# Kernel tuning notes

Hardware: AMD Instinct MI355X
Metric: run time of the kernel (lower is better)

## Reference

```python
import jax, jax.numpy as jnp
import numpy as np

D = 1024      # dim_input
H = 16        # n_heads
DH = 64       # dim_inner
S = 1024      # current_seq
M = 1024      # pre_seq (memory)
B = 2         # batch
SCALE = 1.0 / np.sqrt(DH)


def _rel_shift(x):
    # x: [S, J, B, H]; Transformer-XL relative shift
    s, j = x.shape[0], x.shape[1]
    zero = jnp.zeros((s, 1) + x.shape[2:], x.dtype)
    x = jnp.concatenate([zero, x], axis=1)            # [S, J+1, B, H]
    x = x.reshape((j + 1, s) + x.shape[2:])[1:]        # [J, S, B, H]
    return x.reshape((s, j) + x.shape[2:])             # [S, J, B, H]


def setup_inputs() -> dict:
    key = jax.random.key(0)
    ks = jax.random.split(key, 9)
    std = 1.0 / np.sqrt(D)
    return {
        "multi_head_input": jax.random.normal(ks[0], (S, B, D), jnp.float32),
        "position_emb": jax.random.normal(ks[1], (S + M, D), jnp.float32),
        "memory": jax.random.normal(ks[2], (M, B, D), jnp.float32),
        "u": jax.random.normal(ks[3], (H, DH), jnp.float32) * 0.02,
        "v": jax.random.normal(ks[4], (H, DH), jnp.float32) * 0.02,
        "W_kv": jax.random.normal(ks[5], (D, 2 * H * DH), jnp.float32) * std,
        "W_q": jax.random.normal(ks[6], (D, H * DH), jnp.float32) * std,
        "W_pos": jax.random.normal(ks[7], (D, H * DH), jnp.float32) * std,
        "W_out": jax.random.normal(ks[8], (H * DH, D), jnp.float32) * std,
    }


def reference(multi_head_input, position_emb, memory, u, v, W_kv, W_q, W_pos, W_out):
    s = multi_head_input.shape[0]
    m = memory.shape[0]
    b = multi_head_input.shape[1]
    x_mem = jnp.concatenate([memory, multi_head_input], axis=0)   # [M+S, B, D]
    kv = x_mem @ W_kv                                              # [M+S, B, 2*H*DH]
    k, val = jnp.split(kv, 2, axis=-1)
    k = k.reshape(m + s, b, H, DH)
    val = val.reshape(m + s, b, H, DH)
    q = (multi_head_input @ W_q).reshape(s, b, H, DH)              # [S, B, H, DH]

    # content term: (q + u) . k
    content = jnp.einsum('ibhd,jbhd->ijbh', q + u, k)              # [S, M+S, B, H]
    # position term: (q + v) . r, then rel_shift
    r = (position_emb @ W_pos).reshape(m + s, H, DH)               # [M+S, H, DH]
    pos = jnp.einsum('ibhd,jhd->ijbh', q + v, r)                   # [S, M+S, B, H]
    pos = _rel_shift(pos)

    attn = jax.nn.softmax((content + pos) * SCALE, axis=1)         # [S, M+S, B, H]
    out = jnp.einsum('ijbh,jbhd->ibhd', attn, val).reshape(s, b, H * DH)
    return out @ W_out                                             # [S, B, D]
```

## Files before the change

### kernel.cpp

```cpp
#include <hip/hip_runtime.h>
#include <hip/hip_bf16.h>
#include <hip/hip_fp16.h>
#include <math.h>

#define D    1024
#define H    16
#define DH   64
#define S    1024
#define M    1024
#define B    2
#define J    2048
#define SCALE 0.125f

typedef __attribute__((ext_vector_type(8))) short        bf16x8;
typedef __attribute__((ext_vector_type(4))) short        s16x4;
typedef __attribute__((ext_vector_type(8))) _Float16     h16x8;
typedef __attribute__((ext_vector_type(4))) _Float16     h16x4;
typedef __attribute__((ext_vector_type(8))) unsigned short us8;
typedef __attribute__((ext_vector_type(4))) float        f32x4;

__device__ __forceinline__ short f2bs(float f) {
    __hip_bfloat16 t = __float2bfloat16(f);
    short r; __builtin_memcpy(&r, &t, 2); return r;
}
__device__ __forceinline__ unsigned short f2bf_fast(float f) {
    unsigned int u; __builtin_memcpy(&u, &f, 4);
    return (unsigned short)((u + 0x8000u) >> 16);
}

__device__ __forceinline__ void g2l16(const short* g, short* l) {
    __builtin_amdgcn_global_load_lds(
        (const __attribute__((address_space(1))) unsigned int*)g,
        (__attribute__((address_space(3))) unsigned int*)l, 16, 0, 0);
}

__global__ __launch_bounds__(256)
void prep(const float* __restrict__ mem, const float* __restrict__ x,
          const float* __restrict__ pemb,
          const float* __restrict__ Wkv, const float* __restrict__ Wq,
          const float* __restrict__ Wpos, const float* __restrict__ Wout,
          short* __restrict__ a_bf, short* __restrict__ p_bf,
          short* __restrict__ wkvt, short* __restrict__ wqt,
          short* __restrict__ wpt,  short* __restrict__ wot)
{
    __shared__ float t[64][65];
    int blk = blockIdx.x;
    const int tid = threadIdx.x;
    if (blk < 6144) {
        const int idx = (blk * 256 + tid) * 4;
        const int TWO_M = 2 * 1024 * 1024;
        float4 v; short* dst;
        if (idx < TWO_M)          { v = *(const float4*)(mem  + idx);           dst = a_bf + idx; }
        else if (idx < 2 * TWO_M) { v = *(const float4*)(x    + idx - TWO_M);   dst = a_bf + idx; }
        else                      { v = *(const float4*)(pemb + idx - 2*TWO_M); dst = p_bf + idx - 2*TWO_M; }
        s16x4 o = { f2bs(v.x), f2bs(v.y), f2bs(v.z), f2bs(v.w) };
        *(s16x4*)dst = o;
        return;
    }
    blk -= 6144;
    const float* src; short* dst; int N, t0;
    if (blk < 512)       { src = Wkv;  dst = wkvt; N = 2048; t0 = blk; }
    else if (blk < 768)  { src = Wq;   dst = wqt;  N = 1024; t0 = blk - 512; }
    else if (blk < 1024) { src = Wpos; dst = wpt;  N = 1024; t0 = blk - 768; }
    else                 { src = Wout; dst = wot;  N = 1024; t0 = blk - 1024; }
    const int ntn = N >> 6;
    const int k0 = (t0 / ntn) * 64, n0 = (t0 % ntn) * 64;
    #pragma unroll
    for (int e = tid; e < 4096; e += 256) {
        int r = e >> 6, c = e & 63;
        t[r][c] = src[(size_t)(k0 + r) * N + n0 + c];
    }
    __syncthreads();
    #pragma unroll
    for (int e = tid; e < 4096; e += 256) {
        int nr = e >> 6, kc = e & 63;
        dst[(size_t)(n0 + nr) * 1024 + k0 + kc] = f2bs(t[kc][nr]);
    }
}

__device__ __forceinline__ void gemm_core(const short* __restrict__ A,
                                          const short* __restrict__ Bt,
                                          short* As, short* Bs,
                                          int bm0, int bn0, int tid,
                                          f32x4 acc[4][4])
{
    const int w    = tid >> 6;
    const int wy   = w >> 1, wx = w & 1;
    const int lane = tid & 63;
    const int lm   = lane & 15;
    const int lq   = lane >> 4;

    for (int k0 = 0; k0 < 1024; k0 += 64) {
        const short* Ab = A  + (size_t)bm0 * 1024 + k0;
        const short* Bb = Bt + (size_t)bn0 * 1024 + k0;
        #pragma unroll
        for (int t = 0; t < 4; ++t) {
            int s = t * 256 + tid;
            int r = s >> 3, c = s & 7;
            int cg = c ^ (r & 7);
            g2l16(Ab + r * 1024 + cg * 8, As + s * 8);
            g2l16(Bb + r * 1024 + cg * 8, Bs + s * 8);
        }
        __syncthreads();
        #pragma unroll
        for (int kk = 0; kk < 2; ++kk) {
            bf16x8 af[4], bg[4];
            #pragma unroll
            for (int r4 = 0; r4 < 4; ++r4) {
                int ar = wy * 64 + r4 * 16 + lm;
                int kc = kk * 4 + lq;
                af[r4] = *(const bf16x8*)(As + ((ar << 3) + (kc ^ (ar & 7))) * 8);
            }
            #pragma unroll
            for (int c4 = 0; c4 < 4; ++c4) {
                int br = wx * 64 + c4 * 16 + lm;
                int kc = kk * 4 + lq;
                bg[c4] = *(const bf16x8*)(Bs + ((br << 3) + (kc ^ (br & 7))) * 8);
            }
            #pragma unroll
            for (int r4 = 0; r4 < 4; ++r4)
                #pragma unroll
                for (int c4 = 0; c4 < 4; ++c4)
                    acc[r4][c4] = __builtin_amdgcn_mfma_f32_16x16x32_bf16(
                        af[r4], bg[c4], acc[r4][c4], 0, 0, 0);
        }
        __syncthreads();
    }
}

__global__ __launch_bounds__(256)
void proj_fused(const short* __restrict__ a_bf, const short* __restrict__ p_bf,
                const short* __restrict__ wkvt, const short* __restrict__ wqt,
                const short* __restrict__ wpt,
                short* __restrict__ k_bf, short* __restrict__ vt_bf,
                short* __restrict__ qu_bf, short* __restrict__ qv_bf,
                short* __restrict__ r_bf,
                const float* __restrict__ uvec, const float* __restrict__ vvec)
{
    __shared__ __align__(16) short As[128 * 64];
    __shared__ __align__(16) short Bs[128 * 64];

    int blk = blockIdx.x;
    int mode, bx, by;
    const short *A, *Bt;
    if (blk < 512)      { bx = blk & 15; by = blk >> 4;
                          if (bx >= 8) { mode = 4; A = wkvt; Bt = a_bf; }
                          else         { mode = 0; A = a_bf; Bt = wkvt; } }
    else if (blk < 640) { int b2 = blk - 512; mode = 1; bx = b2 & 7; by = b2 >> 3;
                          A = a_bf + (size_t)2048 * 1024; Bt = wqt; }
    else                { int b3 = blk - 640; mode = 2; bx = b3 & 7; by = b3 >> 3;
                          A = p_bf; Bt = wpt; }
    const int bn0 = (mode == 4) ? by * 128 : bx * 128;
    const int bm0 = (mode == 4) ? bx * 128 : by * 128;
    const int tid = threadIdx.x;
    const int w = tid >> 6, wy = w >> 1, wx = w & 1;
    const int lane = tid & 63, lm = lane & 15, lq = lane >> 4;

    f32x4 acc[4][4];
    #pragma unroll
    for (int r = 0; r < 4; ++r)
        #pragma unroll
        for (int c = 0; c < 4; ++c) acc[r][c] = (f32x4){0.f, 0.f, 0.f, 0.f};

    gemm_core(A, Bt, As, Bs, bm0, bn0, tid, acc);

    #pragma unroll
    for (int r4 = 0; r4 < 4; ++r4) {
        #pragma unroll
        for (int c4 = 0; c4 < 4; ++c4) {
            const int n = bn0 + wx * 64 + c4 * 16 + lm;
            float ubias = 0.f, vbias = 0.f;
            if (mode == 1) { ubias = uvec[n]; vbias = vvec[n]; }
            #pragma unroll
            for (int reg = 0; reg < 4; ++reg) {
                const int m = bm0 + wy * 64 + r4 * 16 + lq * 4 + reg;
                const float val = acc[r4][c4][reg];
                if (mode == 0) {
                    int j = m >> 1, b = m & 1;
                    int h = n >> 6, d = n & 63;
                    k_bf[(((size_t)b * H + h) * J + j) * DH + d] = f2bs(val);
                } else if (mode == 4) {
                    int n2 = m - 1024, h = n2 >> 6, d = n2 & 63;
                    int j = n >> 1, b = n & 1;
                    vt_bf[(((size_t)b * H + h) * DH + d) * J + j] = f2bs(val);
                } else if (mode == 1) {
                    int i = m >> 1, b = m & 1;
                    int h = n >> 6, d = n & 63;
                    size_t o = (((size_t)b * H + h) * S + i) * DH + d;
                    qu_bf[o] = f2bs((val + ubias) * SCALE);
                    qv_bf[o] = f2bs((val + vbias) * SCALE);
                } else {
                    int h = n >> 6, d = n & 63;
                    r_bf[((size_t)h * J + m) * DH + d] = f2bs(val);
                }
            }
        }
    }
}

__global__ __launch_bounds__(256)
void gemm_out(const short* __restrict__ A, const short* __restrict__ Bt,
              float* __restrict__ out)
{
    __shared__ __align__(16) short As[128 * 64];
    __shared__ __align__(16) short Bs[128 * 64];
    const int bn0 = blockIdx.x * 128, bm0 = blockIdx.y * 128;
    const int tid = threadIdx.x;
    const int w = tid >> 6, wy = w >> 1, wx = w & 1;
    const int lane = tid & 63, lm = lane & 15, lq = lane >> 4;

    f32x4 acc[4][4];
    #pragma unroll
    for (int r = 0; r < 4; ++r)
        #pragma unroll
        for (int c = 0; c < 4; ++c) acc[r][c] = (f32x4){0.f, 0.f, 0.f, 0.f};

    gemm_core(A, Bt, As, Bs, bm0, bn0, tid, acc);

    #pragma unroll
    for (int r4 = 0; r4 < 4; ++r4)
        #pragma unroll
        for (int c4 = 0; c4 < 4; ++c4) {
            const int n = bn0 + wx * 64 + c4 * 16 + lm;
            #pragma unroll
            for (int reg = 0; reg < 4; ++reg) {
                const int m = bm0 + wy * 64 + r4 * 16 + lq * 4 + reg;
                out[(size_t)m * 1024 + n] = acc[r4][c4][reg];
            }
        }
}

__device__ __forceinline__ int sidx(int m, int c) {
    return (m << 10) + (c ^ (m << 3));
}

__global__ __launch_bounds__(512)
void attn_mfma(const short* __restrict__ qu_bf, const short* __restrict__ qv_bf,
               const short* __restrict__ k_bf,  const short* __restrict__ vt_bf,
               const short* __restrict__ r_bf,
               float* __restrict__ opart, float* __restrict__ ml)
{
    __shared__ unsigned short sc[32 * 1024];
    __half* sch = (__half*)sc;
    float*  scF = (float*)sc;

    const int bh  = blockIdx.x;
    const int it  = blockIdx.y;
    const int jh  = blockIdx.z;
    const int i0  = it * 32;
    const int cbeg = jh << 10, cend = cbeg + 1024;
    const int h   = bh & (H - 1);
    const int tid = threadIdx.x;
    const int w    = tid >> 6;
    const int lane = tid & 63;
    const int lm   = lane & 15;
    const int lq   = lane >> 4;
    const int slot = (it * 32 + bh) * 2 + jh;

    const short* qup0 = qu_bf + ((size_t)(bh * S + i0 + lm)) * DH + lq * 8;
    const short* qup1 = qup0 + 16 * DH;
    bf16x8 au00 = *(const bf16x8*)qup0,        au01 = *(const bf16x8*)(qup0 + 32);
    bf16x8 au10 = *(const bf16x8*)qup1,        au11 = *(const bf16x8*)(qup1 + 32);
    const short* qvp0 = qv_bf + ((size_t)(bh * S + i0 + lm)) * DH + lq * 8;
    const short* qvp1 = qvp0 + 16 * DH;
    bf16x8 av00 = *(const bf16x8*)qvp0,        av01 = *(const bf16x8*)(qvp0 + 32);
    bf16x8 av10 = *(const bf16x8*)qvp1,        av11 = *(const bf16x8*)(qvp1 + 32);
    int r1a = i0 + 1 + lm;  if (r1a > S - 1) r1a = S - 1;
    int r1b = i0 + 17 + lm; if (r1b > S - 1) r1b = S - 1;
    const short* qwp0 = qv_bf + ((size_t)(bh * S + r1a)) * DH + lq * 8;
    const short* qwp1 = qv_bf + ((size_t)(bh * S + r1b)) * DH + lq * 8;
    bf16x8 aw00 = *(const bf16x8*)qwp0,        aw01 = *(const bf16x8*)(qwp0 + 32);
    bf16x8 aw10 = *(const bf16x8*)qwp1,        aw11 = *(const bf16x8*)(qwp1 + 32);

    if (tid < 32) {
        int hole = i0 + tid + 1025;
        if (hole >= cbeg && hole < cend) sc[sidx(tid, hole - cbeg)] = 0;
    }

    const short* rbase = r_bf + (size_t)h * J * DH;

    {
        int tmp = cbeg + 977 - i0;
        int tlo = tmp > 0 ? ((tmp + 15) >> 4) : 0;
        int thi = (cend + 1022 - i0) >> 4; if (thi > 127) thi = 127;
        int t = tlo + w;
        if (t <= thi) {
            const short* rp = rbase + (size_t)(t * 16 + lm) * DH + lq * 8;
            bf16x8 b0 = *(const bf16x8*)rp, b1 = *(const bf16x8*)(rp + 32);
            for (; t <= thi; t += 8) {
                bf16x8 n0, n1;
                if (t + 8 <= thi) {
                    const short* rpn = rbase + (size_t)((t + 8) * 16 + lm) * DH + lq * 8;
                    n0 = *(const bf16x8*)rpn; n1 = *(const bf16x8*)(rpn + 32);
                }
                f32x4 c0 = {0.f,0.f,0.f,0.f}, c1 = {0.f,0.f,0.f,0.f};
                c0 = __builtin_amdgcn_mfma_f32_16x16x32_bf16(av00, b0, c0, 0, 0, 0);
                c1 = __builtin_amdgcn_mfma_f32_16x16x32_bf16(av10, b0, c1, 0, 0, 0);
                c0 = __builtin_amdgcn_mfma_f32_16x16x32_bf16(av01, b1, c0, 0, 0, 0);
                c1 = __builtin_amdgcn_mfma_f32_16x16x32_bf16(av11, b1, c1, 0, 0, 0);
                int cb = i0 + t * 16 + lm - 1023 - cbeg;
                int base = i0 + 16 * t - 1023;
                if (base >= cbeg && base + 46 < cend) {
                    #pragma unroll
                    for (int r = 0; r < 4; ++r) {
                        int m0 = lq * 4 + r, m1 = m0 + 16;
                        sch[sidx(m0, cb + m0)] = __float2half(c0[r]);
                        sch[sidx(m1, cb + m1)] = __float2half(c1[r]);
                    }
                } else {
                    #pragma unroll
                    for (int r = 0; r < 4; ++r) {
                        int m0 = lq * 4 + r, m1 = m0 + 16;
                        int cA = cb + m0, cB = cb + m1;
                        if (cA >= 0 && cA < 1024) sch[sidx(m0, cA)] = __float2half(c0[r]);
                        if (cB >= 0 && cB < 1024) sch[sidx(m1, cB)] = __float2half(c1[r]);
                    }
                }
                b0 = n0; b1 = n1;
            }
        }
    }

    {
        int tmpw = cbeg - 1072 - i0;
        int tlw = tmpw > 0 ? ((tmpw + 15) >> 4) : 0;
        int thw = (cend - 1027 - i0) >> 4; if (thw > 127) thw = 127;
        int t = tlw + w;
        if (t <= thw) {
            const short* rp = rbase + (size_t)(t * 16 + lm) * DH + lq * 8;
            bf16x8 b0 = *(const bf16x8*)rp, b1 = *(const bf16x8*)(rp + 32);
            for (; t <= thw; t += 8) {
                bf16x8 n0, n1;
                if (t + 8 <= thw) {
                    const short* rpn = rbase + (size_t)((t + 8) * 16 + lm) * DH + lq * 8;
                    n0 = *(const bf16x8*)rpn; n1 = *(const bf16x8*)(rpn + 32);
                }
                f32x4 c0 = {0.f,0.f,0.f,0.f}, c1 = {0.f,0.f,0.f,0.f};
                c0 = __builtin_amdgcn_mfma_f32_16x16x32_bf16(aw00, b0, c0, 0, 0, 0);
                c1 = __builtin_amdgcn_mfma_f32_16x16x32_bf16(aw10, b0, c1, 0, 0, 0);
                c0 = __builtin_amdgcn_mfma_f32_16x16x32_bf16(aw01, b1, c0, 0, 0, 0);
                c1 = __builtin_amdgcn_mfma_f32_16x16x32_bf16(aw11, b1, c1, 0, 0, 0);
                int cb = i0 + t * 16 + lm + 1026 - cbeg;
                int base = i0 + 16 * t + 1026;
                if (base >= cbeg && base + 46 < cend) {
                    #pragma unroll
                    for (int r = 0; r < 4; ++r) {
                        int m0 = lq * 4 + r, m1 = m0 + 16;
                        sch[sidx(m0, cb + m0)] = __float2half(c0[r]);
                        sch[sidx(m1, cb + m1)] = __float2half(c1[r]);
                    }
                } else {
                    #pragma unroll
                    for (int r = 0; r < 4; ++r) {
                        int m0 = lq * 4 + r, m1 = m0 + 16;
                        int cA = cb + m0, cB = cb + m1;
                        if (cA >= 0 && cA < 1024) sch[sidx(m0, cA)] = __float2half(c0[r]);
                        if (cB >= 0 && cB < 1024) sch[sidx(m1, cB)] = __float2half(c1[r]);
                    }
                }
                b0 = n0; b1 = n1;
            }
        }
    }

    const short* kbase = k_bf + (size_t)bh * J * DH;
    int tc0 = jh * 64 + w + 8 * (it & 7);
    const short* kp0 = kbase + (size_t)(tc0 * 16 + lm) * DH + lq * 8;
    bf16x8 kb0 = *(const bf16x8*)kp0, kb1 = *(const bf16x8*)(kp0 + 32);
    __syncthreads();

    #pragma unroll 1
    for (int g = 0; g < 8; ++g) {
        bf16x8 nb0, nb1;
        if (g + 1 < 8) {
            int u = jh * 64 + w + 8 * ((g + 1 + it) & 7);
            const short* np = kbase + (size_t)(u * 16 + lm) * DH + lq * 8;
            nb0 = *(const bf16x8*)np; nb1 = *(const bf16x8*)(np + 32);
        }
        int t = jh * 64 + w + 8 * ((g + it) & 7);
        int lc = t * 16 - cbeg;
        int aA = sidx(lm,      lc + lq * 4);
        int aB = sidx(lm + 16, lc + lq * 4);
        h16x4 hA = *(const h16x4*)(sc + aA);
        h16x4 hB = *(const h16x4*)(sc + aB);
        f32x4 c0, c1;
        #pragma unroll
        for (int r = 0; r < 4; ++r) { c0[r] = (float)hA[r]; c1[r] = (float)hB[r]; }
        c0 = __builtin_amdgcn_mfma_f32_16x16x32_bf16(kb0, au00, c0, 0, 0, 0);
        c1 = __builtin_amdgcn_mfma_f32_16x16x32_bf16(kb0, au10, c1, 0, 0, 0);
        c0 = __builtin_amdgcn_mfma_f32_16x16x32_bf16(kb1, au01, c0, 0, 0, 0);
        c1 = __builtin_amdgcn_mfma_f32_16x16x32_bf16(kb1, au11, c1, 0, 0, 0);
        h16x4 oA, oB;
        #pragma unroll
        for (int r = 0; r < 4; ++r) { oA[r] = (_Float16)c0[r]; oB[r] = (_Float16)c1[r]; }
        *(h16x4*)(sc + aA) = oA;
        *(h16x4*)(sc + aB) = oB;
        kb0 = nb0; kb1 = nb1;
    }

    const int dslice = w & 3, jq = w >> 2;
    const short* vtb = vt_bf + ((size_t)bh * DH + dslice * 16 + lm) * J + cbeg + jq * 512;
    bf16x8 cv0, cv1, cv2, cv3;
    {
        int j0 = (it & 3) * 128;
        cv0 = *(const bf16x8*)(vtb + j0 +  0 + lq * 8);
        cv1 = *(const bf16x8*)(vtb + j0 + 32 + lq * 8);
        cv2 = *(const bf16x8*)(vtb + j0 + 64 + lq * 8);
        cv3 = *(const bf16x8*)(vtb + j0 + 96 + lq * 8);
    }
    __syncthreads();

    {
        const int row = tid >> 4;
        const int cw  = (tid & 15) * 8;
        float ssum = 0.f;
        #pragma unroll
        for (int c = cw; c < 1024; c += 128) {
            int idx = sidx(row, c);
            h16x8 v = *(const h16x8*)(sc + idx);
            us8 e;
            #pragma unroll
            for (int k = 0; k < 8; ++k) {
                float ex = __builtin_amdgcn_exp2f((float)v[k] * 1.44269504f);
                ssum += ex;
                e[k] = f2bf_fast(ex);
            }
            *(us8*)(sc + idx) = e;
        }
        #pragma unroll
        for (int off = 1; off < 16; off <<= 1) ssum += __shfl_xor(ssum, off);
        if ((tid & 15) == 0) {
            ml[(size_t)slot * 64 + row * 2]     = 0.f;
            ml[(size_t)slot * 64 + row * 2 + 1] = ssum;
        }
    }
    __syncthreads();

    f32x4 pa0 = {0.f,0.f,0.f,0.f}, pa1 = {0.f,0.f,0.f,0.f};
    f32x4 pa2 = {0.f,0.f,0.f,0.f}, pa3 = {0.f,0.f,0.f,0.f};
    f32x4 pb0 = {0.f,0.f,0.f,0.f}, pb1 = {0.f,0.f,0.f,0.f};
    f32x4 pb2 = {0.f,0.f,0.f,0.f}, pb3 = {0.f,0.f,0.f,0.f};
    #pragma unroll 1
    for (int jo0 = 0; jo0 < 4; ++jo0) {
        bf16x8 nv0, nv1, nv2, nv3;
        if (jo0 < 3) {
            int jn = ((jo0 + 1 + it) & 3) * 128;
            nv0 = *(const bf16x8*)(vtb + jn +  0 + lq * 8);
            nv1 = *(const bf16x8*)(vtb + jn + 32 + lq * 8);
            nv2 = *(const bf16x8*)(vtb + jn + 64 + lq * 8);
            nv3 = *(const bf16x8*)(vtb + jn + 96 + lq * 8);
        }
        int j0 = ((jo0 + it) & 3) * 128;
        int lb = jq * 512 + j0;
        bf16x8 a0 = *(const bf16x8*)(sc + sidx(lm, lb +  0 + lq * 8));
        bf16x8 a1 = *(const bf16x8*)(sc + sidx(lm, lb + 32 + lq * 8));
        bf16x8 a2 = *(const bf16x8*)(sc + sidx(lm, lb + 64 + lq * 8));
        bf16x8 a3 = *(const bf16x8*)(sc + sidx(lm, lb + 96 + lq * 8));
        bf16x8 c0 = *(const bf16x8*)(sc + sidx(16 + lm, lb +  0 + lq * 8));
        bf16x8 c1 = *(const bf16x8*)(sc + sidx(16 + lm, lb + 32 + lq * 8));
        bf16x8 c2 = *(const bf16x8*)(sc + sidx(16 + lm, lb + 64 + lq * 8));
        bf16x8 c3 = *(const bf16x8*)(sc + sidx(16 + lm, lb + 96 + lq * 8));
        pa0 = __builtin_amdgcn_mfma_f32_16x16x32_bf16(a0, cv0, pa0, 0, 0, 0);
        pb0 = __builtin_amdgcn_mfma_f32_16x16x32_bf16(c0, cv0, pb0, 0, 0, 0);
        pa1 = __builtin_amdgcn_mfma_f32_16x16x32_bf16(a1, cv1, pa1, 0, 0, 0);
        pb1 = __builtin_amdgcn_mfma_f32_16x16x32_bf16(c1, cv1, pb1, 0, 0, 0);
        pa2 = __builtin_amdgcn_mfma_f32_16x16x32_bf16(a2, cv2, pa2, 0, 0, 0);
        pb2 = __builtin_amdgcn_mfma_f32_16x16x32_bf16(c2, cv2, pb2, 0, 0, 0);
        pa3 = __builtin_amdgcn_mfma_f32_16x16x32_bf16(a3, cv3, pa3, 0, 0, 0);
        pb3 = __builtin_amdgcn_mfma_f32_16x16x32_bf16(c3, cv3, pb3, 0, 0, 0);
        if (jo0 < 3) { cv0 = nv0; cv1 = nv1; cv2 = nv2; cv3 = nv3; }
    }
    __syncthreads();

    #pragma unroll
    for (int r = 0; r < 4; ++r) {
        int m0 = lq * 4 + r, m1 = m0 + 16;
        scF[jq * 2048 + m0 * 64 + dslice * 16 + lm] = pa0[r] + pa1[r] + pa2[r] + pa3[r];
        scF[jq * 2048 + m1 * 64 + dslice * 16 + lm] = pb0[r] + pb1[r] + pb2[r] + pb3[r];
    }
    __syncthreads();

    float* op = opart + (size_t)slot * 2048;
    #pragma unroll
    for (int e = tid; e < 2048; e += 512)
        op[e] = scF[e] + scF[2048 + e];
}

__global__ __launch_bounds__(256)
void attn_combine(const float* __restrict__ opart, const float* __restrict__ ml,
                  short* __restrict__ o_bf)
{
    const int blk = blockIdx.x;
    const int it = blk >> 5, bh = blk & 31;
    const int h = bh & 15, b = bh >> 4;
    __shared__ float wgt[32][2];
    const int tid = threadIdx.x;
    if (tid < 32) {
        float m0 = ml[(size_t)(blk * 2 + 0) * 64 + tid * 2];
        float l0 = ml[(size_t)(blk * 2 + 0) * 64 + tid * 2 + 1];
        float m1 = ml[(size_t)(blk * 2 + 1) * 64 + tid * 2];
        float l1 = ml[(size_t)(blk * 2 + 1) * 64 + tid * 2 + 1];
        float mx = fmaxf(m0, m1);
        float e0 = __expf(m0 - mx), e1 = __expf(m1 - mx);
        float inv = 1.0f / (e0 * l0 + e1 * l1);
        wgt[tid][0] = e0 * inv;
        wgt[tid][1] = e1 * inv;
    }
    __syncthreads();
    const float* p0 = opart + (size_t)(blk * 2 + 0) * 2048;
    const float* p1 = opart + (size_t)(blk * 2 + 1) * 2048;
    #pragma unroll
    for (int e = tid; e < 2048; e += 256) {
        int m = e >> 6, d = e & 63;
        float val = p0[e] * wgt[m][0] + p1[e] * wgt[m][1];
        o_bf[((size_t)(it * 32 + m) * B + b) * (H * DH) + h * DH + d] = f2bs(val);
    }
}

extern "C" void kernel_launch(void* const* d_in, const int* in_sizes, int n_in,
                              void* d_out, int out_size, void* d_ws, size_t ws_size,
                              hipStream_t stream)
{
    const float* x    = (const float*)d_in[0];
    const float* pemb = (const float*)d_in[1];
    const float* mem  = (const float*)d_in[2];
    const float* u    = (const float*)d_in[3];
    const float* v    = (const float*)d_in[4];
    const float* Wkv  = (const float*)d_in[5];
    const float* Wq   = (const float*)d_in[6];
    const float* Wpos = (const float*)d_in[7];
    const float* Wout = (const float*)d_in[8];
    float* out = (float*)d_out;

    char* p = (char*)d_ws;
    short* a_bf  = (short*)p; p += (size_t)4096 * 1024 * 2;
    short* p_bf  = (short*)p; p += (size_t)2048 * 1024 * 2;
    short* wkvt  = (short*)p; p += (size_t)2048 * 1024 * 2;
    short* wqt   = (short*)p; p += (size_t)1024 * 1024 * 2;
    short* wpt   = (short*)p; p += (size_t)1024 * 1024 * 2;
    short* wot   = (short*)p; p += (size_t)1024 * 1024 * 2;
    short* k_bf  = (short*)p; p += (size_t)B * H * J * DH * 2;
    short* vt_bf = (short*)p; p += (size_t)B * H * J * DH * 2;
    short* qu_bf = (short*)p; p += (size_t)B * H * S * DH * 2;
    short* qv_bf = (short*)p; p += (size_t)B * H * S * DH * 2;
    short* r_bf  = (short*)p; p += (size_t)H * J * DH * 2;
    short* o_bf  = (short*)p;

    float* opart = (float*)d_ws;
    float* ml    = (float*)((char*)d_ws + (size_t)16 * 1024 * 1024);

    prep<<<7424, 256, 0, stream>>>(mem, x, pemb, Wkv, Wq, Wpos, Wout,
                                   a_bf, p_bf, wkvt, wqt, wpt, wot);
    proj_fused<<<768, 256, 0, stream>>>(a_bf, p_bf, wkvt, wqt, wpt,
                                        k_bf, vt_bf, qu_bf, qv_bf, r_bf, u, v);
    attn_mfma<<<dim3(B * H, S / 32, 2), 512, 0, stream>>>(
        qu_bf, qv_bf, k_bf, vt_bf, r_bf, opart, ml);
    attn_combine<<<(S / 32) * B * H, 256, 0, stream>>>(opart, ml, o_bf);
    gemm_out<<<dim3(8, 16), 256, 0, stream>>>(o_bf, wot, out);
}
```

Measured before the change: 296.4 us.

## Process attention key range in two 512-column chunks to halve score LDS

New measurement: 320.6 us. 1.08x slower.

```diff
diff --git a/kernel.cpp b/kernel.cpp
--- a/kernel.cpp
+++ b/kernel.cpp
@@ -231,7 +231,7 @@
 }
 
 __device__ __forceinline__ int sidx(int m, int c) {
-    return (m << 10) + (c ^ (m << 3));
+    return (m << 9) + (c ^ (m << 3));
 }
 
 __global__ __launch_bounds__(512)
@@ -240,15 +240,14 @@
                const short* __restrict__ r_bf,
                float* __restrict__ opart, float* __restrict__ ml)
 {
-    __shared__ unsigned short sc[32 * 1024];
+    __shared__ __align__(16) unsigned short sc[32 * 512];
+    __shared__ __align__(16) float oacc[4096];
     __half* sch = (__half*)sc;
-    float*  scF = (float*)sc;
 
     const int bh  = blockIdx.x;
     const int it  = blockIdx.y;
     const int jh  = blockIdx.z;
     const int i0  = it * 32;
-    const int cbeg = jh << 10, cend = cbeg + 1024;
     const int h   = bh & (H - 1);
     const int tid = threadIdx.x;
     const int w    = tid >> 6;
@@ -256,234 +255,259 @@
     const int lm   = lane & 15;
     const int lq   = lane >> 4;
     const int slot = (it * 32 + bh) * 2 + jh;
-
-    const short* qup0 = qu_bf + ((size_t)(bh * S + i0 + lm)) * DH + lq * 8;
-    const short* qup1 = qup0 + 16 * DH;
-    bf16x8 au00 = *(const bf16x8*)qup0,        au01 = *(const bf16x8*)(qup0 + 32);
-    bf16x8 au10 = *(const bf16x8*)qup1,        au11 = *(const bf16x8*)(qup1 + 32);
-    const short* qvp0 = qv_bf + ((size_t)(bh * S + i0 + lm)) * DH + lq * 8;
-    const short* qvp1 = qvp0 + 16 * DH;
-    bf16x8 av00 = *(const bf16x8*)qvp0,        av01 = *(const bf16x8*)(qvp0 + 32);
-    bf16x8 av10 = *(const bf16x8*)qvp1,        av11 = *(const bf16x8*)(qvp1 + 32);
-    int r1a = i0 + 1 + lm;  if (r1a > S - 1) r1a = S - 1;
-    int r1b = i0 + 17 + lm; if (r1b > S - 1) r1b = S - 1;
-    const short* qwp0 = qv_bf + ((size_t)(bh * S + r1a)) * DH + lq * 8;
-    const short* qwp1 = qv_bf + ((size_t)(bh * S + r1b)) * DH + lq * 8;
-    bf16x8 aw00 = *(const bf16x8*)qwp0,        aw01 = *(const bf16x8*)(qwp0 + 32);
-    bf16x8 aw10 = *(const bf16x8*)qwp1,        aw11 = *(const bf16x8*)(qwp1 + 32);
-
-    if (tid < 32) {
-        int hole = i0 + tid + 1025;
-        if (hole >= cbeg && hole < cend) sc[sidx(tid, hole - cbeg)] = 0;
-    }
+    const int dslice = w & 3, jq = w >> 2;
 
     const short* rbase = r_bf + (size_t)h * J * DH;
+    const short* kbase = k_bf + (size_t)bh * J * DH;
+
+    float ssum = 0.f;
+
+    #pragma unroll 1
+    for (int ch = 0; ch < 2; ++ch) {
+        const int cbeg = (jh << 10) + (ch << 9);
+        const int cend = cbeg + 512;
+
+        const short* qvp0 = qv_bf + ((size_t)(bh * S + i0 + lm)) * DH + lq * 8;
+        const short* qvp1 = qvp0 + 16 * DH;
+        bf16x8 av00 = *(const bf16x8*)qvp0, av01 = *(const bf16x8*)(qvp0 + 32);
+        bf16x8 av10 = *(const bf16x8*)qvp1, av11 = *(const bf16x8*)(qvp1 + 32);
+        int r1a = i0 + 1 + lm;  if (r1a > S - 1) r1a = S - 1;
+        int r1b = i0 + 17 + lm; if (r1b > S - 1) r1b = S - 1;
+        const short* qwp0 = qv_bf + ((size_t)(bh * S + r1a)) * DH + lq * 8;
+        const short* qwp1 = qv_bf + ((size_t)(bh * S + r1b)) * DH + lq * 8;
+        bf16x8 aw00 = *(const bf16x8*)qwp0, aw01 = *(const bf16x8*)(qwp0 + 32);
+        bf16x8 aw10 = *(const bf16x8*)qwp1, aw11 = *(const bf16x8*)(qwp1 + 32);
+
+        if (tid < 32) {
+            int hole = i0 + tid + 1025;
+            if (hole >= cbeg && hole < cend) sc[sidx(tid, hole - cbeg)] = 0;
+        }
+
+        {
+            int tmp = cbeg + 977 - i0;
+            int tlo = tmp > 0 ? ((tmp + 15) >> 4) : 0;
+            int thi = (cend + 1022 - i0) >> 4; if (thi > 127) thi = 127;
+            int t = tlo + w;
+            if (t <= thi) {
+                const short* rp = rbase + (size_t)(t * 16 + lm) * DH + lq * 8;
+                bf16x8 b0 = *(const bf16x8*)rp, b1 = *(const bf16x8*)(rp + 32);
+                for (; t <= thi; t += 8) {
+                    bf16x8 n0, n1;
+                    if (t + 8 <= thi) {
+                        const short* rpn = rbase + (size_t)((t + 8) * 16 + lm) * DH + lq * 8;
+                        n0 = *(const bf16x8*)rpn; n1 = *(const bf16x8*)(rpn + 32);
+                    }
+                    f32x4 c0 = {0.f,0.f,0.f,0.f}, c1 = {0.f,0.f,0.f,0.f};
+                    c0 = __builtin_amdgcn_mfma_f32_16x16x32_bf16(av00, b0, c0, 0, 0, 0);
+                    c1 = __builtin_amdgcn_mfma_f32_16x16x32_bf16(av10, b0, c1, 0, 0, 0);
+                    c0 = __builtin_amdgcn_mfma_f32_16x16x32_bf16(av01, b1, c0, 0, 0, 0);
+                    c1 = __builtin_amdgcn_mfma_f32_16x16x32_bf16(av11, b1, c1, 0, 0, 0);
+                    int cb = i0 + t * 16 + lm - 1023 - cbeg;
+                    int base = i0 + 16 * t - 1023;
+                    if (base >= cbeg && base + 46 < cend) {
+                        #pragma unroll
+                        for (int r = 0; r < 4; ++r) {
+                            int m0 = lq * 4 + r, m1 = m0 + 16;
+                            sch[sidx(m0, cb + m0)] = __float2half(c0[r]);
+                            sch[sidx(m1, cb + m1)] = __float2half(c1[r]);
+                        }
+                    } else {
+                        #pragma unroll
+                        for (int r = 0; r < 4; ++r) {
+                            int m0 = lq * 4 + r, m1 = m0 + 16;
+                            int cA = cb + m0, cB = cb + m1;
+                            if (cA >= 0 && cA < 512) sch[sidx(m0, cA)] = __float2half(c0[r]);
+                            if (cB >= 0 && cB < 512) sch[sidx(m1, cB)] = __float2half(c1[r]);
+                        }
+                    }
+                    b0 = n0; b1 = n1;
+                }
+            }
+        }
+
+        {
+            int tmpw = cbeg - 1072 - i0;
+            int tlw = tmpw > 0 ? ((tmpw + 15) >> 4) : 0;
+            int thw = (cend - 1027 - i0) >> 4; if (thw > 127) thw = 127;
+            int t = tlw + w;
+            if (t <= thw) {
+                const short* rp = rbase + (size_t)(t * 16 + lm) * DH + lq * 8;
+                bf16x8 b0 = *(const bf16x8*)rp, b1 = *(const bf16x8*)(rp + 32);
+                for (; t <= thw; t += 8) {
+                    bf16x8 n0, n1;
+                    if (t + 8 <= thw) {
+                        const short* rpn = rbase + (size_t)((t + 8) * 16 + lm) * DH + lq * 8;
+                        n0 = *(const bf16x8*)rpn; n1 = *(const bf16x8*)(rpn + 32);
+                    }
+                    f32x4 c0 = {0.f,0.f,0.f,0.f}, c1 = {0.f,0.f,0.f,0.f};
+                    c0 = __builtin_amdgcn_mfma_f32_16x16x32_bf16(aw00, b0, c0, 0, 0, 0);
+                    c1 = __builtin_amdgcn_mfma_f32_16x16x32_bf16(aw10, b0, c1, 0, 0, 0);
+                    c0 = __builtin_amdgcn_mfma_f32_16x16x32_bf16(aw01, b1, c0, 0, 0, 0);
+                    c1 = __builtin_amdgcn_mfma_f32_16x16x32_bf16(aw11, b1, c1, 0, 0, 0);
+                    int cb = i0 + t * 16 + lm + 1026 - cbeg;
+                    int base = i0 + 16 * t + 1026;
+                    if (base >= cbeg && base + 46 < cend) {
+                        #pragma unroll
+                        for (int r = 0; r < 4; ++r) {
+                            int m0 = lq * 4 + r, m1 = m0 + 16;
+                            sch[sidx(m0, cb + m0)] = __float2half(c0[r]);
+                            sch[sidx(m1, cb + m1)] = __float2half(c1[r]);
+                        }
+                    } else {
+                        #pragma unroll
+                        for (int r = 0; r < 4; ++r) {
+                            int m0 = lq * 4 + r, m1 = m0 + 16;
+                            int cA = cb + m0, cB = cb + m1;
+                            if (cA >= 0 && cA < 512) sch[sidx(m0, cA)] = __float2half(c0[r]);
+                            if (cB >= 0 && cB < 512) sch[sidx(m1, cB)] = __float2half(c1[r]);
+                        }
+                    }
+                    b0 = n0; b1 = n1;
+                }
+            }
+        }
+
+        const int tb = cbeg >> 4;
+        bf16x8 kb0, kb1;
+        {
+            int t0 = tb + w + 8 * (it & 3);
+            const short* kp0 = kbase + (size_t)(t0 * 16 + lm) * DH + lq * 8;
+            kb0 = *(const bf16x8*)kp0; kb1 = *(const bf16x8*)(kp0 + 32);
+        }
+        __syncthreads();
+
+        const short* qup0 = qu_bf + ((size_t)(bh * S + i0 + lm)) * DH + lq * 8;
+        const short* qup1 = qup0 + 16 * DH;
+        bf16x8 au00 = *(const bf16x8*)qup0, au01 = *(const bf16x8*)(qup0 + 32);
+        bf16x8 au10 = *(const bf16x8*)qup1, au11 = *(const bf16x8*)(qup1 + 32);
+
+        #pragma unroll 1
+        for (int g = 0; g < 4; ++g) {
+            bf16x8 nb0, nb1;
+            if (g + 1 < 4) {
+                int u = tb + w + 8 * ((g + 1 + it) & 3);
+                const short* np = kbase + (size_t)(u * 16 + lm) * DH + lq * 8;
+                nb0 = *(const bf16x8*)np; nb1 = *(const bf16x8*)(np + 32);
+            }
+            int t = tb + w + 8 * ((g + it) & 3);
+            int lc = (t << 4) - cbeg;
+            int aA = sidx(lm,      lc + lq * 4);
+            int aB = sidx(lm + 16, lc + lq * 4);
+            h16x4 hA = *(const h16x4*)(sc + aA);
+            h16x4 hB = *(const h16x4*)(sc + aB);
+            f32x4 c0, c1;
+            #pragma unroll
+            for (int r = 0; r < 4; ++r) { c0[r] = (float)hA[r]; c1[r] = (float)hB[r]; }
+            c0 = __builtin_amdgcn_mfma_f32_16x16x32_bf16(kb0, au00, c0, 0, 0, 0);
+            c1 = __builtin_amdgcn_mfma_f32_16x16x32_bf16(kb0, au10, c1, 0, 0, 0);
+            c0 = __builtin_amdgcn_mfma_f32_16x16x32_bf16(kb1, au01, c0, 0, 0, 0);
+            c1 = __builtin_amdgcn_mfma_f32_16x16x32_bf16(kb1, au11, c1, 0, 0, 0);
+            h16x4 oA, oB;
+            #pragma unroll
+            for (int r = 0; r < 4; ++r) { oA[r] = (_Float16)c0[r]; oB[r] = (_Float16)c1[r]; }
+            *(h16x4*)(sc + aA) = oA;
+            *(h16x4*)(sc + aB) = oB;
+            kb0 = nb0; kb1 = nb1;
+        }
+
+        const short* vtb = vt_bf + ((size_t)bh * DH + dslice * 16 + lm) * J + cbeg + jq * 256;
+        bf16x8 cv0, cv1, cv2, cv3;
+        {
+            int j0 = (it & 1) * 128;
+            cv0 = *(const bf16x8*)(vtb + j0 +  0 + lq * 8);
+            cv1 = *(const bf16x8*)(vtb + j0 + 32 + lq * 8);
+            cv2 = *(const bf16x8*)(vtb + j0 + 64 + lq * 8);
+            cv3 = *(const bf16x8*)(vtb + j0 + 96 + lq * 8);
+        }
+        __syncthreads();
+
+        {
+            const int row = tid >> 4;
+            const int cw  = (tid & 15) * 8;
+            #pragma unroll
+            for (int c = cw; c < 512; c += 128) {
+                int idx = sidx(row, c);
+                h16x8 v = *(const h16x8*)(sc + idx);
+                us8 e;
+                #pragma unroll
+                for (int k = 0; k < 8; ++k) {
+                    float ex = __builtin_amdgcn_exp2f((float)v[k] * 1.44269504f);
+                    ssum += ex;
+                    e[k] = f2bf_fast(ex);
+                }
+                *(us8*)(sc + idx) = e;
+            }
+        }
+        __syncthreads();
+
+        f32x4 pa0 = {0.f,0.f,0.f,0.f}, pa1 = {0.f,0.f,0.f,0.f};
+        f32x4 pa2 = {0.f,0.f,0.f,0.f}, pa3 = {0.f,0.f,0.f,0.f};
+        f32x4 pb0 = {0.f,0.f,0.f,0.f}, pb1 = {0.f,0.f,0.f,0.f};
+        f32x4 pb2 = {0.f,0.f,0.f,0.f}, pb3 = {0.f,0.f,0.f,0.f};
+        #pragma unroll 1
+        for (int jo0 = 0; jo0 < 2; ++jo0) {
+            bf16x8 nv0, nv1, nv2, nv3;
+            if (jo0 < 1) {
+                int jn = ((jo0 + 1 + it) & 1) * 128;
+                nv0 = *(const bf16x8*)(vtb + jn +  0 + lq * 8);
+                nv1 = *(const bf16x8*)(vtb + jn + 32 + lq * 8);
+                nv2 = *(const bf16x8*)(vtb + jn + 64 + lq * 8);
+                nv3 = *(const bf16x8*)(vtb + jn + 96 + lq * 8);
+            }
+            int j0 = ((jo0 + it) & 1) * 128;
+            int lb = jq * 256 + j0;
+            bf16x8 a0 = *(const bf16x8*)(sc + sidx(lm, lb +  0 + lq * 8));
+            bf16x8 a1 = *(const bf16x8*)(sc + sidx(lm, lb + 32 + lq * 8));
+            bf16x8 a2 = *(const bf16x8*)(sc + sidx(lm, lb + 64 + lq * 8));
+            bf16x8 a3 = *(const bf16x8*)(sc + sidx(lm, lb + 96 + lq * 8));
+            bf16x8 c0 = *(const bf16x8*)(sc + sidx(16 + lm, lb +  0 + lq * 8));
+            bf16x8 c1 = *(const bf16x8*)(sc + sidx(16 + lm, lb + 32 + lq * 8));
+            bf16x8 c2 = *(const bf16x8*)(sc + sidx(16 + lm, lb + 64 + lq * 8));
+            bf16x8 c3 = *(const bf16x8*)(sc + sidx(16 + lm, lb + 96 + lq * 8));
+            pa0 = __builtin_amdgcn_mfma_f32_16x16x32_bf16(a0, cv0, pa0, 0, 0, 0);
+            pb0 = __builtin_amdgcn_mfma_f32_16x16x32_bf16(c0, cv0, pb0, 0, 0, 0);
+            pa1 = __builtin_amdgcn_mfma_f32_16x16x32_bf16(a1, cv1, pa1, 0, 0, 0);
+            pb1 = __builtin_amdgcn_mfma_f32_16x16x32_bf16(c1, cv1, pb1, 0, 0, 0);
+            pa2 = __builtin_amdgcn_mfma_f32_16x16x32_bf16(a2, cv2, pa2, 0, 0, 0);
+            pb2 = __builtin_amdgcn_mfma_f32_16x16x32_bf16(c2, cv2, pb2, 0, 0, 0);
+            pa3 = __builtin_amdgcn_mfma_f32_16x16x32_bf16(a3, cv3, pa3, 0, 0, 0);
+            pb3 = __builtin_amdgcn_mfma_f32_16x16x32_bf16(c3, cv3, pb3, 0, 0, 0);
+            if (jo0 < 1) { cv0 = nv0; cv1 = nv1; cv2 = nv2; cv3 = nv3; }
+        }
+
+        if (ch == 0) {
+            #pragma unroll
+            for (int r = 0; r < 4; ++r) {
+                int m0 = lq * 4 + r, m1 = m0 + 16;
+                oacc[jq * 2048 + m0 * 64 + dslice * 16 + lm] = pa0[r] + pa1[r] + pa2[r] + pa3[r];
+                oacc[jq * 2048 + m1 * 64 + dslice * 16 + lm] = pb0[r] + pb1[r] + pb2[r] + pb3[r];
+            }
+        } else {
+            #pragma unroll
+            for (int r = 0; r < 4; ++r) {
+                int m0 = lq * 4 + r, m1 = m0 + 16;
+                oacc[jq * 2048 + m0 * 64 + dslice * 16 + lm] += pa0[r] + pa1[r] + pa2[r] + pa3[r];
+                oacc[jq * 2048 + m1 * 64 + dslice * 16 + lm] += pb0[r] + pb1[r] + pb2[r] + pb3[r];
+            }
+        }
+        __syncthreads();
+    }
 
     {
-        int tmp = cbeg + 977 - i0;
-        int tlo = tmp > 0 ? ((tmp + 15) >> 4) : 0;
-        int thi = (cend + 1022 - i0) >> 4; if (thi > 127) thi = 127;
-        int t = tlo + w;
-        if (t <= thi) {
-            const short* rp = rbase + (size_t)(t * 16 + lm) * DH + lq * 8;
-            bf16x8 b0 = *(const bf16x8*)rp, b1 = *(const bf16x8*)(rp + 32);
-            for (; t <= thi; t += 8) {
-                bf16x8 n0, n1;
-                if (t + 8 <= thi) {
-                    const short* rpn = rbase + (size_t)((t + 8) * 16 + lm) * DH + lq * 8;
-                    n0 = *(const bf16x8*)rpn; n1 = *(const bf16x8*)(rpn + 32);
-                }
-                f32x4 c0 = {0.f,0.f,0.f,0.f}, c1 = {0.f,0.f,0.f,0.f};
-                c0 = __builtin_amdgcn_mfma_f32_16x16x32_bf16(av00, b0, c0, 0, 0, 0);
-                c1 = __builtin_amdgcn_mfma_f32_16x16x32_bf16(av10, b0, c1, 0, 0, 0);
-                c0 = __builtin_amdgcn_mfma_f32_16x16x32_bf16(av01, b1, c0, 0, 0, 0);
-                c1 = __builtin_amdgcn_mfma_f32_16x16x32_bf16(av11, b1, c1, 0, 0, 0);
-                int cb = i0 + t * 16 + lm - 1023 - cbeg;
-                int base = i0 + 16 * t - 1023;
-                if (base >= cbeg && base + 46 < cend) {
-                    #pragma unroll
-                    for (int r = 0; r < 4; ++r) {
-                        int m0 = lq * 4 + r, m1 = m0 + 16;
-                        sch[sidx(m0, cb + m0)] = __float2half(c0[r]);
-                        sch[sidx(m1, cb + m1)] = __float2half(c1[r]);
-                    }
-                } else {
-                    #pragma unroll
-                    for (int r = 0; r < 4; ++r) {
-                        int m0 = lq * 4 + r, m1 = m0 + 16;
-                        int cA = cb + m0, cB = cb + m1;
-                        if (cA >= 0 && cA < 1024) sch[sidx(m0, cA)] = __float2half(c0[r]);
-                        if (cB >= 0 && cB < 1024) sch[sidx(m1, cB)] = __float2half(c1[r]);
-                    }
-                }
-                b0 = n0; b1 = n1;
-            }
-        }
-    }
-
-    {
-        int tmpw = cbeg - 1072 - i0;
-        int tlw = tmpw > 0 ? ((tmpw + 15) >> 4) : 0;
-        int thw = (cend - 1027 - i0) >> 4; if (thw > 127) thw = 127;
-        int t = tlw + w;
-        if (t <= thw) {
-            const short* rp = rbase + (size_t)(t * 16 + lm) * DH + lq * 8;
-            bf16x8 b0 = *(const bf16x8*)rp, b1 = *(const bf16x8*)(rp + 32);
-            for (; t <= thw; t += 8) {
-                bf16x8 n0, n1;
-                if (t + 8 <= thw) {
-                    const short* rpn = rbase + (size_t)((t + 8) * 16 + lm) * DH + lq * 8;
-                    n0 = *(const bf16x8*)rpn; n1 = *(const bf16x8*)(rpn + 32);
-                }
-                f32x4 c0 = {0.f,0.f,0.f,0.f}, c1 = {0.f,0.f,0.f,0.f};
-                c0 = __builtin_amdgcn_mfma_f32_16x16x32_bf16(aw00, b0, c0, 0, 0, 0);
-                c1 = __builtin_amdgcn_mfma_f32_16x16x32_bf16(aw10, b0, c1, 0, 0, 0);
-                c0 = __builtin_amdgcn_mfma_f32_16x16x32_bf16(aw01, b1, c0, 0, 0, 0);
-                c1 = __builtin_amdgcn_mfma_f32_16x16x32_bf16(aw11, b1, c1, 0, 0, 0);
-                int cb = i0 + t * 16 + lm + 1026 - cbeg;
-                int base = i0 + 16 * t + 1026;
-                if (base >= cbeg && base + 46 < cend) {
-                    #pragma unroll
-                    for (int r = 0; r < 4; ++r) {
-                        int m0 = lq * 4 + r, m1 = m0 + 16;
-                        sch[sidx(m0, cb + m0)] = __float2half(c0[r]);
-                        sch[sidx(m1, cb + m1)] = __float2half(c1[r]);
-                    }
-                } else {
-                    #pragma unroll
-                    for (int r = 0; r < 4; ++r) {
-                        int m0 = lq * 4 + r, m1 = m0 + 16;
-                        int cA = cb + m0, cB = cb + m1;
-                        if (cA >= 0 && cA < 1024) sch[sidx(m0, cA)] = __float2half(c0[r]);
-                        if (cB >= 0 && cB < 1024) sch[sidx(m1, cB)] = __float2half(c1[r]);
-                    }
-                }
-                b0 = n0; b1 = n1;
-            }
-        }
-    }
-
-    const short* kbase = k_bf + (size_t)bh * J * DH;
-    int tc0 = jh * 64 + w + 8 * (it & 7);
-    const short* kp0 = kbase + (size_t)(tc0 * 16 + lm) * DH + lq * 8;
-    bf16x8 kb0 = *(const bf16x8*)kp0, kb1 = *(const bf16x8*)(kp0 + 32);
-    __syncthreads();
-
-    #pragma unroll 1
-    for (int g = 0; g < 8; ++g) {
-        bf16x8 nb0, nb1;
-        if (g + 1 < 8) {
-            int u = jh * 64 + w + 8 * ((g + 1 + it) & 7);
-            const short* np = kbase + (size_t)(u * 16 + lm) * DH + lq * 8;
-            nb0 = *(const bf16x8*)np; nb1 = *(const bf16x8*)(np + 32);
-        }
-        int t = jh * 64 + w + 8 * ((g + it) & 7);
-        int lc = t * 16 - cbeg;
-        int aA = sidx(lm,      lc + lq * 4);
-        int aB = sidx(lm + 16, lc + lq * 4);
-        h16x4 hA = *(const h16x4*)(sc + aA);
-        h16x4 hB = *(const h16x4*)(sc + aB);
-        f32x4 c0, c1;
-        #pragma unroll
-        for (int r = 0; r < 4; ++r) { c0[r] = (float)hA[r]; c1[r] = (float)hB[r]; }
-        c0 = __builtin_amdgcn_mfma_f32_16x16x32_bf16(kb0, au00, c0, 0, 0, 0);
-        c1 = __builtin_amdgcn_mfma_f32_16x16x32_bf16(kb0, au10, c1, 0, 0, 0);
-        c0 = __builtin_amdgcn_mfma_f32_16x16x32_bf16(kb1, au01, c0, 0, 0, 0);
-        c1 = __builtin_amdgcn_mfma_f32_16x16x32_bf16(kb1, au11, c1, 0, 0, 0);
-        h16x4 oA, oB;
-        #pragma unroll
-        for (int r = 0; r < 4; ++r) { oA[r] = (_Float16)c0[r]; oB[r] = (_Float16)c1[r]; }
-        *(h16x4*)(sc + aA) = oA;
-        *(h16x4*)(sc + aB) = oB;
-        kb0 = nb0; kb1 = nb1;
-    }
-
-    const int dslice = w & 3, jq = w >> 2;
-    const short* vtb = vt_bf + ((size_t)bh * DH + dslice * 16 + lm) * J + cbeg + jq * 512;
-    bf16x8 cv0, cv1, cv2, cv3;
-    {
-        int j0 = (it & 3) * 128;
-        cv0 = *(const bf16x8*)(vtb + j0 +  0 + lq * 8);
-        cv1 = *(const bf16x8*)(vtb + j0 + 32 + lq * 8);
-        cv2 = *(const bf16x8*)(vtb + j0 + 64 + lq * 8);
-        cv3 = *(const bf16x8*)(vtb + j0 + 96 + lq * 8);
-    }
-    __syncthreads();
-
-    {
+        float s = ssum;
+        #pragma unroll
+        for (int off = 1; off < 16; off <<= 1) s += __shfl_xor(s, off);
         const int row = tid >> 4;
-        const int cw  = (tid & 15) * 8;
-        float ssum = 0.f;
-        #pragma unroll
-        for (int c = cw; c < 1024; c += 128) {
-            int idx = sidx(row, c);
-            h16x8 v = *(const h16x8*)(sc + idx);
-            us8 e;
-            #pragma unroll
-            for (int k = 0; k < 8; ++k) {
-                float ex = __builtin_amdgcn_exp2f((float)v[k] * 1.44269504f);
-                ssum += ex;
-                e[k] = f2bf_fast(ex);
-            }
-            *(us8*)(sc + idx) = e;
-        }
-        #pragma unroll
-        for (int off = 1; off < 16; off <<= 1) ssum += __shfl_xor(ssum, off);
         if ((tid & 15) == 0) {
             ml[(size_t)slot * 64 + row * 2]     = 0.f;
-            ml[(size_t)slot * 64 + row * 2 + 1] = ssum;
-        }
-    }
-    __syncthreads();
-
-    f32x4 pa0 = {0.f,0.f,0.f,0.f}, pa1 = {0.f,0.f,0.f,0.f};
-    f32x4 pa2 = {0.f,0.f,0.f,0.f}, pa3 = {0.f,0.f,0.f,0.f};
-    f32x4 pb0 = {0.f,0.f,0.f,0.f}, pb1 = {0.f,0.f,0.f,0.f};
-    f32x4 pb2 = {0.f,0.f,0.f,0.f}, pb3 = {0.f,0.f,0.f,0.f};
-    #pragma unroll 1
-    for (int jo0 = 0; jo0 < 4; ++jo0) {
-        bf16x8 nv0, nv1, nv2, nv3;
-        if (jo0 < 3) {
-            int jn = ((jo0 + 1 + it) & 3) * 128;
-            nv0 = *(const bf16x8*)(vtb + jn +  0 + lq * 8);
-            nv1 = *(const bf16x8*)(vtb + jn + 32 + lq * 8);
-            nv2 = *(const bf16x8*)(vtb + jn + 64 + lq * 8);
-            nv3 = *(const bf16x8*)(vtb + jn + 96 + lq * 8);
-        }
-        int j0 = ((jo0 + it) & 3) * 128;
-        int lb = jq * 512 + j0;
-        bf16x8 a0 = *(const bf16x8*)(sc + sidx(lm, lb +  0 + lq * 8));
-        bf16x8 a1 = *(const bf16x8*)(sc + sidx(lm, lb + 32 + lq * 8));
-        bf16x8 a2 = *(const bf16x8*)(sc + sidx(lm, lb + 64 + lq * 8));
-        bf16x8 a3 = *(const bf16x8*)(sc + sidx(lm, lb + 96 + lq * 8));
-        bf16x8 c0 = *(const bf16x8*)(sc + sidx(16 + lm, lb +  0 + lq * 8));
-        bf16x8 c1 = *(const bf16x8*)(sc + sidx(16 + lm, lb + 32 + lq * 8));
-        bf16x8 c2 = *(const bf16x8*)(sc + sidx(16 + lm, lb + 64 + lq * 8));
-        bf16x8 c3 = *(const bf16x8*)(sc + sidx(16 + lm, lb + 96 + lq * 8));
-        pa0 = __builtin_amdgcn_mfma_f32_16x16x32_bf16(a0, cv0, pa0, 0, 0, 0);
-        pb0 = __builtin_amdgcn_mfma_f32_16x16x32_bf16(c0, cv0, pb0, 0, 0, 0);
-        pa1 = __builtin_amdgcn_mfma_f32_16x16x32_bf16(a1, cv1, pa1, 0, 0, 0);
-        pb1 = __builtin_amdgcn_mfma_f32_16x16x32_bf16(c1, cv1, pb1, 0, 0, 0);
-        pa2 = __builtin_amdgcn_mfma_f32_16x16x32_bf16(a2, cv2, pa2, 0, 0, 0);
-        pb2 = __builtin_amdgcn_mfma_f32_16x16x32_bf16(c2, cv2, pb2, 0, 0, 0);
-        pa3 = __builtin_amdgcn_mfma_f32_16x16x32_bf16(a3, cv3, pa3, 0, 0, 0);
-        pb3 = __builtin_amdgcn_mfma_f32_16x16x32_bf16(c3, cv3, pb3, 0, 0, 0);
-        if (jo0 < 3) { cv0 = nv0; cv1 = nv1; cv2 = nv2; cv3 = nv3; }
-    }
-    __syncthreads();
-
-    #pragma unroll
-    for (int r = 0; r < 4; ++r) {
-        int m0 = lq * 4 + r, m1 = m0 + 16;
-        scF[jq * 2048 + m0 * 64 + dslice * 16 + lm] = pa0[r] + pa1[r] + pa2[r] + pa3[r];
-        scF[jq * 2048 + m1 * 64 + dslice * 16 + lm] = pb0[r] + pb1[r] + pb2[r] + pb3[r];
-    }
-    __syncthreads();
+            ml[(size_t)slot * 64 + row * 2 + 1] = s;
+        }
+    }
 
     float* op = opart + (size_t)slot * 2048;
     #pragma unroll
     for (int e = tid; e < 2048; e += 512)
-        op[e] = scF[e] + scF[2048 + e];
+        op[e] = oacc[e] + oacc[2048 + e];
 }
 
 __global__ __launch_bounds__(256)
```

## Deepen attention prefetch, fold log2e into Q scale, remap blocks per XCD

Applied to the files above, without the earlier changes.

New measurement: 293.6 us. About the same (-0.9%).

```diff
diff --git a/kernel.cpp b/kernel.cpp
--- a/kernel.cpp
+++ b/kernel.cpp
@@ -11,6 +11,7 @@
 #define B    2
 #define J    2048
 #define SCALE 0.125f
+#define SCALE_L2E 0.18033688f
 
 typedef __attribute__((ext_vector_type(8))) short        bf16x8;
 typedef __attribute__((ext_vector_type(4))) short        s16x4;
@@ -187,8 +188,8 @@
                     int i = m >> 1, b = m & 1;
                     int h = n >> 6, d = n & 63;
                     size_t o = (((size_t)b * H + h) * S + i) * DH + d;
-                    qu_bf[o] = f2bs((val + ubias) * SCALE);
-                    qv_bf[o] = f2bs((val + vbias) * SCALE);
+                    qu_bf[o] = f2bs((val + ubias) * SCALE_L2E);
+                    qv_bf[o] = f2bs((val + vbias) * SCALE_L2E);
                 } else {
                     int h = n >> 6, d = n & 63;
                     r_bf[((size_t)h * J + m) * DH + d] = f2bs(val);
@@ -244,9 +245,14 @@
     __half* sch = (__half*)sc;
     float*  scF = (float*)sc;
 
-    const int bh  = blockIdx.x;
-    const int it  = blockIdx.y;
-    const int jh  = blockIdx.z;
+    const int L   = blockIdx.x;
+    const int xcd = L & 7;
+    const int pp  = L >> 3;
+    const int bh  = (xcd << 2) + (pp >> 6);
+    const int sub = pp & 63;
+    const int it  = sub >> 1;
+    const int jh  = sub & 1;
+
     const int i0  = it * 32;
     const int cbeg = jh << 10, cend = cbeg + 1024;
     const int h   = bh & (H - 1);
@@ -287,10 +293,15 @@
         if (t <= thi) {
             const short* rp = rbase + (size_t)(t * 16 + lm) * DH + lq * 8;
             bf16x8 b0 = *(const bf16x8*)rp, b1 = *(const bf16x8*)(rp + 32);
+            bf16x8 p0, p1;
+            if (t + 8 <= thi) {
+                const short* rp2 = rbase + (size_t)((t + 8) * 16 + lm) * DH + lq * 8;
+                p0 = *(const bf16x8*)rp2; p1 = *(const bf16x8*)(rp2 + 32);
+            }
             for (; t <= thi; t += 8) {
                 bf16x8 n0, n1;
-                if (t + 8 <= thi) {
-                    const short* rpn = rbase + (size_t)((t + 8) * 16 + lm) * DH + lq * 8;
+                if (t + 16 <= thi) {
+                    const short* rpn = rbase + (size_t)((t + 16) * 16 + lm) * DH + lq * 8;
                     n0 = *(const bf16x8*)rpn; n1 = *(const bf16x8*)(rpn + 32);
                 }
                 f32x4 c0 = {0.f,0.f,0.f,0.f}, c1 = {0.f,0.f,0.f,0.f};
@@ -316,7 +327,7 @@
                         if (cB >= 0 && cB < 1024) sch[sidx(m1, cB)] = __float2half(c1[r]);
                     }
                 }
-                b0 = n0; b1 = n1;
+                b0 = p0; b1 = p1; p0 = n0; p1 = n1;
             }
         }
     }
@@ -329,10 +340,15 @@
         if (t <= thw) {
             const short* rp = rbase + (size_t)(t * 16 + lm) * DH + lq * 8;
             bf16x8 b0 = *(const bf16x8*)rp, b1 = *(const bf16x8*)(rp + 32);
+            bf16x8 p0, p1;
+            if (t + 8 <= thw) {
+                const short* rp2 = rbase + (size_t)((t + 8) * 16 + lm) * DH + lq * 8;
+                p0 = *(const bf16x8*)rp2; p1 = *(const bf16x8*)(rp2 + 32);
+            }
             for (; t <= thw; t += 8) {
                 bf16x8 n0, n1;
-                if (t + 8 <= thw) {
-                    const short* rpn = rbase + (size_t)((t + 8) * 16 + lm) * DH + lq * 8;
+                if (t + 16 <= thw) {
+                    const short* rpn = rbase + (size_t)((t + 16) * 16 + lm) * DH + lq * 8;
                     n0 = *(const bf16x8*)rpn; n1 = *(const bf16x8*)(rpn + 32);
                 }
                 f32x4 c0 = {0.f,0.f,0.f,0.f}, c1 = {0.f,0.f,0.f,0.f};
@@ -358,22 +374,28 @@
                         if (cB >= 0 && cB < 1024) sch[sidx(m1, cB)] = __float2half(c1[r]);
                     }
                 }
-                b0 = n0; b1 = n1;
+                b0 = p0; b1 = p1; p0 = n0; p1 = n1;
             }
         }
     }
 
     const short* kbase = k_bf + (size_t)bh * J * DH;
-    int tc0 = jh * 64 + w + 8 * (it & 7);
-    const short* kp0 = kbase + (size_t)(tc0 * 16 + lm) * DH + lq * 8;
-    bf16x8 kb0 = *(const bf16x8*)kp0, kb1 = *(const bf16x8*)(kp0 + 32);
+    bf16x8 kb0, kb1, kc0, kc1;
+    {
+        int t0 = jh * 64 + w + 8 * ((it) & 7);
+        int t1 = jh * 64 + w + 8 * ((1 + it) & 7);
+        const short* kp0 = kbase + (size_t)(t0 * 16 + lm) * DH + lq * 8;
+        const short* kp1 = kbase + (size_t)(t1 * 16 + lm) * DH + lq * 8;
+        kb0 = *(const bf16x8*)kp0; kb1 = *(const bf16x8*)(kp0 + 32);
+        kc0 = *(const bf16x8*)kp1; kc1 = *(const bf16x8*)(kp1 + 32);
+    }
     __syncthreads();
 
     #pragma unroll 1
     for (int g = 0; g < 8; ++g) {
         bf16x8 nb0, nb1;
-        if (g + 1 < 8) {
-            int u = jh * 64 + w + 8 * ((g + 1 + it) & 7);
+        if (g + 2 < 8) {
+            int u = jh * 64 + w + 8 * ((g + 2 + it) & 7);
             const short* np = kbase + (size_t)(u * 16 + lm) * DH + lq * 8;
             nb0 = *(const bf16x8*)np; nb1 = *(const bf16x8*)(np + 32);
         }
@@ -395,7 +417,7 @@
         for (int r = 0; r < 4; ++r) { oA[r] = (_Float16)c0[r]; oB[r] = (_Float16)c1[r]; }
         *(h16x4*)(sc + aA) = oA;
         *(h16x4*)(sc + aB) = oB;
-        kb0 = nb0; kb1 = nb1;
+        kb0 = kc0; kb1 = kc1; kc0 = nb0; kc1 = nb1;
     }
 
     const int dslice = w & 3, jq = w >> 2;
@@ -421,7 +443,7 @@
             us8 e;
             #pragma unroll
             for (int k = 0; k < 8; ++k) {
-                float ex = __builtin_amdgcn_exp2f((float)v[k] * 1.44269504f);
+                float ex = __builtin_amdgcn_exp2f((float)v[k]);
                 ssum += ex;
                 e[k] = f2bf_fast(ex);
             }
@@ -553,7 +575,7 @@
                                    a_bf, p_bf, wkvt, wqt, wpt, wot);
     proj_fused<<<768, 256, 0, stream>>>(a_bf, p_bf, wkvt, wqt, wpt,
                                         k_bf, vt_bf, qu_bf, qv_bf, r_bf, u, v);
-    attn_mfma<<<dim3(B * H, S / 32, 2), 512, 0, stream>>>(
+    attn_mfma<<<2048, 512, 0, stream>>>(
         qu_bf, qv_bf, k_bf, vt_bf, r_bf, opart, ml);
     attn_combine<<<(S / 32) * B * H, 256, 0, stream>>>(opart, ml, o_bf);
     gemm_out<<<dim3(8, 16), 256, 0, stream>>>(o_bf, wot, out);
```
